# Performance work log

Hardware: AMD Instinct MI355X
Metric: run time of the kernel (lower is better)

The kernel has to match this reference:

```python
import jax, jax.numpy as jnp
import numpy as np
import math

B, L, DM, H, NREL, VS = 16, 512, 512, 8, 4, 5
DK = DM // H


def setup_inputs() -> dict:
    key = jax.random.key(0)
    ks = jax.random.split(key, 16)
    s = 1.0 / math.sqrt(DM)
    inp = {
        'query': jax.random.normal(ks[0], (B, L, DM), jnp.float32),
        'key': jax.random.normal(ks[1], (B, L, DM), jnp.float32),
        'value': jax.random.normal(ks[2], (B, L, DM), jnp.float32),
        'rel_mat': jax.random.randint(ks[3], (B, NREL, L, L), 0, VS),
        'mask': jnp.ones((B, L, L), dtype=bool),
        'Wq': jax.random.normal(ks[4], (DM, DM), jnp.float32) * s,
        'bq': jnp.zeros((DM,), jnp.float32),
        'Wk': jax.random.normal(ks[5], (DM, DM), jnp.float32) * s,
        'bk': jnp.zeros((DM,), jnp.float32),
        'Wv': jax.random.normal(ks[6], (DM, DM), jnp.float32) * s,
        'bv': jnp.zeros((DM,), jnp.float32),
        'Wo': jax.random.normal(ks[7], (DM, DM), jnp.float32) * s,
        'bo': jnp.zeros((DM,), jnp.float32),
    }
    # relation embeddings: (n_rel, h, vs, d_k), padding_idx=0 rows are zero
    se = jax.random.normal(ks[8], (NREL, H, VS, DK), jnp.float32) * 0.02
    ve = jax.random.normal(ks[9], (NREL, H, VS, DK), jnp.float32) * 0.02
    inp['score_emb'] = se.at[:, :, 0, :].set(0.0)
    inp['value_emb'] = ve.at[:, :, 0, :].set(0.0)
    return inp


def reference(query, key, value, rel_mat, mask, Wq, bq, Wk, bk, Wv, bv, Wo, bo, score_emb, value_emb):
    b, l, dm = query.shape
    n_rel, h, vs, dk = score_emb.shape
    scale = 1.0 / math.sqrt(dk)

    def proj(x, W, bias):
        # (b, l, dm) -> (b, h, l, dk)
        return (x @ W.T + bias).reshape(b, l, h, dk).transpose(0, 2, 1, 3)

    q = proj(query, Wq, bq)
    k = proj(key, Wk, bk)
    v = proj(value, Wv, bv)

    # relative-position score: gather q.emb^T along vocab axis by rel_mat
    rps = jnp.einsum('bhid,rhvd->rbhiv', q, score_emb) * scale  # (r,b,h,l,vs)
    idx = jnp.broadcast_to(rel_mat.transpose(1, 0, 2, 3)[:, :, None], (n_rel, b, h, l, l))
    rel_score = jnp.take_along_axis(rps, idx, axis=-1).sum(0)  # (b,h,l,l)

    scores = jnp.einsum('bhid,bhjd->bhij', q, k) * scale + rel_score
    scores = jnp.where(mask[:, None], scores, -1e9)
    p_attn = jax.nn.softmax(scores, axis=-1)  # (b,h,l,l)

    x = jnp.einsum('bhij,bhjd->bhid', p_attn, v)

    # relative-position value: accumulate attention mass per relation id (skip pad id 0)
    one_hot = jax.nn.one_hot(rel_mat, vs, dtype=p_attn.dtype)  # (b,r,l,l,vs)
    acm = jnp.einsum('bhij,brijs->brhis', p_attn, one_hot)[..., 1:]  # (b,r,h,l,vs-1)
    x = x + jnp.einsum('brhis,rhsd->bhid', acm, value_emb[:, :, 1:])

    out = x.transpose(0, 2, 1, 3).reshape(b, l, dm) @ Wo.T + bo
    return out
```

## Files before the change

kernel.cpp:

```cpp
#include <hip/hip_runtime.h>

#define B_    16
#define L_    512
#define DM_   512
#define H_    8
#define DK_   64
#define NREL_ 4
#define VS_   5

typedef __bf16 bf16x8 __attribute__((ext_vector_type(8)));
typedef float  f32x4  __attribute__((ext_vector_type(4)));

union U64 { uint2 u; long l; };

__device__ __forceinline__ void split1(float x, unsigned short& h, unsigned short& l) {
    unsigned u = __float_as_uint(x);
    h = (unsigned short)(u >> 16);
    float r = x - __uint_as_float(u & 0xffff0000u);
    l = (unsigned short)(__float_as_uint(r) >> 16);
}
__device__ __forceinline__ unsigned bf16rtne(float f) {
    unsigned u = __float_as_uint(f);
    return (u + 0x7fffu + ((u >> 16) & 1u)) >> 16;
}

__global__ __launch_bounds__(256) void conv_w(
    const float* __restrict__ W0, const float* __restrict__ W1,
    const float* __restrict__ W2, const float* __restrict__ W3,
    unsigned short* __restrict__ hi, unsigned short* __restrict__ lo)
{
    const int which = blockIdx.y;
    const float* src = (which == 0) ? W0 : (which == 1) ? W1 : (which == 2) ? W2 : W3;
    int t = blockIdx.x * 256 + threadIdx.x;
    float4 v = ((const float4*)src)[t];
    ushort4 h4, l4;
    split1(v.x, h4.x, l4.x); split1(v.y, h4.y, l4.y);
    split1(v.z, h4.z, l4.z); split1(v.w, h4.w, l4.w);
    ((ushort4*)(hi + (size_t)which * 262144))[t] = h4;
    ((ushort4*)(lo + (size_t)which * 262144))[t] = l4;
}

__global__ __launch_bounds__(256) void pack_rel(
    const int* __restrict__ rel, unsigned short* __restrict__ relp)
{
    int t = blockIdx.x * 256 + threadIdx.x;
    int b = t >> 16;
    int ij4 = t & 65535;
    const int4* rb = (const int4*)(rel + (size_t)b * 4 * 262144) + ij4;
    int4 r0 = rb[0];
    int4 r1 = rb[65536];
    int4 r2 = rb[131072];
    int4 r3 = rb[196608];
    ushort4 o;
    o.x = (unsigned short)(r0.x | (r1.x << 3) | (r2.x << 6) | (r3.x << 9));
    o.y = (unsigned short)(r0.y | (r1.y << 3) | (r2.y << 6) | (r3.y << 9));
    o.z = (unsigned short)(r0.z | (r1.z << 3) | (r2.z << 6) | (r3.z << 9));
    o.w = (unsigned short)(r0.w | (r1.w << 3) | (r2.w << 6) | (r3.w << 9));
    ((ushort4*)relp)[t] = o;
}

template <int A_SPLIT, int MODE>
__device__ __forceinline__ void gemm_core(
    const float* __restrict__ A32,
    const unsigned short* __restrict__ Ahi_g, const unsigned short* __restrict__ Alo_g,
    const unsigned short* __restrict__ Whi_g, const unsigned short* __restrict__ Wlo_g,
    const float* __restrict__ bias,
    float* __restrict__ out_f, unsigned short* __restrict__ out_h,
    unsigned short* __restrict__ out_l)
{
    extern __shared__ __align__(16) char smem[];
    unsigned short* Ah = (unsigned short*)smem;
    unsigned short* Al = Ah + 128 * 40;
    unsigned short* Wh = Al + 128 * 40;
    unsigned short* Wl = Wh + 128 * 40;

    const int tid = threadIdx.x;
    const int lane = tid & 63, wave = tid >> 6;
    const int wm = (wave & 1) << 6, wn = (wave >> 1) << 6;
    const int fr = lane & 15, fq = lane >> 4, koff = fq << 3;
    const int mb = blockIdx.x << 7, nb = blockIdx.y << 7;

    f32x4 acc[4][4];
#pragma unroll
    for (int i = 0; i < 4; i++)
#pragma unroll
        for (int j = 0; j < 4; j++) acc[i][j] = (f32x4){0.f, 0.f, 0.f, 0.f};

    for (int k0 = 0; k0 < 512; k0 += 32) {
        __syncthreads();
#pragma unroll
        for (int it = 0; it < 2; ++it) {
            int idx = tid + (it << 8);
            int r = idx >> 2, c8 = (idx & 3) << 3;
            *(uint4*)&Wh[r * 40 + c8] = *(const uint4*)&Whi_g[(size_t)(nb + r) * 512 + k0 + c8];
            *(uint4*)&Wl[r * 40 + c8] = *(const uint4*)&Wlo_g[(size_t)(nb + r) * 512 + k0 + c8];
        }
        if (A_SPLIT) {
#pragma unroll
            for (int it = 0; it < 2; ++it) {
                int idx = tid + (it << 8);
                int r = idx >> 2, c8 = (idx & 3) << 3;
                *(uint4*)&Ah[r * 40 + c8] = *(const uint4*)&Ahi_g[(size_t)(mb + r) * 512 + k0 + c8];
                *(uint4*)&Al[r * 40 + c8] = *(const uint4*)&Alo_g[(size_t)(mb + r) * 512 + k0 + c8];
            }
        } else {
#pragma unroll
            for (int it = 0; it < 4; ++it) {
                int idx = tid + (it << 8);
                int r = idx >> 3, c4 = (idx & 7) << 2;
                float4 v = *(const float4*)&A32[(size_t)(mb + r) * 512 + k0 + c4];
                unsigned ux = __float_as_uint(v.x), uy = __float_as_uint(v.y);
                unsigned uz = __float_as_uint(v.z), uw = __float_as_uint(v.w);
                unsigned h01 = __builtin_amdgcn_perm(uy, ux, 0x07060302u);
                unsigned h23 = __builtin_amdgcn_perm(uw, uz, 0x07060302u);
                float rx = v.x - __uint_as_float(ux & 0xffff0000u);
                float ry = v.y - __uint_as_float(uy & 0xffff0000u);
                float rz = v.z - __uint_as_float(uz & 0xffff0000u);
                float rw = v.w - __uint_as_float(uw & 0xffff0000u);
                unsigned l01 = __builtin_amdgcn_perm(__float_as_uint(ry), __float_as_uint(rx), 0x07060302u);
                unsigned l23 = __builtin_amdgcn_perm(__float_as_uint(rw), __float_as_uint(rz), 0x07060302u);
                uint2 hw; hw.x = h01; hw.y = h23;
                uint2 lw; lw.x = l01; lw.y = l23;
                *(uint2*)&Ah[r * 40 + c4] = hw;
                *(uint2*)&Al[r * 40 + c4] = lw;
            }
        }
        __syncthreads();

        bf16x8 ah[4], al[4], bh[4], bl[4];
#pragma unroll
        for (int i = 0; i < 4; i++) {
            ah[i] = *(const bf16x8*)&Ah[(wm + (i << 4) + fr) * 40 + koff];
            al[i] = *(const bf16x8*)&Al[(wm + (i << 4) + fr) * 40 + koff];
            bh[i] = *(const bf16x8*)&Wh[(wn + (i << 4) + fr) * 40 + koff];
            bl[i] = *(const bf16x8*)&Wl[(wn + (i << 4) + fr) * 40 + koff];
        }
#pragma unroll
        for (int mi = 0; mi < 4; mi++)
#pragma unroll
            for (int ni = 0; ni < 4; ni++) {
                acc[mi][ni] = __builtin_amdgcn_mfma_f32_16x16x32_bf16(al[mi], bh[ni], acc[mi][ni], 0, 0, 0);
                acc[mi][ni] = __builtin_amdgcn_mfma_f32_16x16x32_bf16(ah[mi], bl[ni], acc[mi][ni], 0, 0, 0);
                acc[mi][ni] = __builtin_amdgcn_mfma_f32_16x16x32_bf16(ah[mi], bh[ni], acc[mi][ni], 0, 0, 0);
            }
    }
    __syncthreads();

    if (MODE == 0) {
        float* epf = (float*)smem;
#pragma unroll
        for (int pass = 0; pass < 2; pass++) {
            if (pass) __syncthreads();
            if (wm == pass * 64) {
#pragma unroll
                for (int ni = 0; ni < 4; ni++) {
                    float bv = bias[nb + wn + (ni << 4) + fr];
#pragma unroll
                    for (int mi = 0; mi < 4; mi++)
#pragma unroll
                        for (int r = 0; r < 4; r++)
                            epf[((mi << 4) + (fq << 2) + r) * 132 + wn + (ni << 4) + fr]
                                = acc[mi][ni][r] + bv;
                }
            }
            __syncthreads();
#pragma unroll
            for (int p = 0; p < 8; p++) {
                int slot = tid + (p << 8);
                int row = slot >> 5, seg = slot & 31;
                int m = mb + pass * 64 + row;
                *(float4*)&out_f[(size_t)m * 512 + nb + (seg << 2)]
                    = *(const float4*)&epf[row * 132 + (seg << 2)];
            }
        }
    } else if (MODE == 1) {
        unsigned short* ep = (unsigned short*)smem;
#pragma unroll
        for (int pass = 0; pass < 2; pass++) {
            if (pass) __syncthreads();
#pragma unroll
            for (int ni = 0; ni < 4; ni++) {
                float bv = bias[nb + wn + (ni << 4) + fr];
#pragma unroll
                for (int mi = 0; mi < 4; mi++)
#pragma unroll
                    for (int r = 0; r < 4; r++) {
                        float val = acc[mi][ni][r] + bv;
                        unsigned short hv, lv;
                        split1(val, hv, lv);
                        ep[(wm + (mi << 4) + (fq << 2) + r) * 136 + wn + (ni << 4) + fr]
                            = pass ? lv : hv;
                    }
            }
            __syncthreads();
            unsigned short* dst = pass ? out_l : out_h;
#pragma unroll
            for (int p = 0; p < 8; p++) {
                int slot = tid + (p << 8);
                int row = slot >> 4, seg = slot & 15;
                int m = mb + row, colg = nb + (seg << 3);
                int bb = m >> 9, ii = m & 511, hh = colg >> 6, dd = colg & 63;
                size_t idx = (((size_t)(bb << 3) + hh) * 512 + ii) * 64 + dd;
                *(uint4*)&dst[idx] = *(const uint4*)&ep[row * 136 + (seg << 3)];
            }
        }
    } else {
        unsigned short* ep = (unsigned short*)smem;
#pragma unroll
        for (int ni = 0; ni < 4; ni++) {
            float bv = bias[nb + wn + (ni << 4) + fr];
#pragma unroll
            for (int mi = 0; mi < 4; mi++)
#pragma unroll
                for (int r = 0; r < 4; r++)
                    ep[(wm + (mi << 4) + (fq << 2) + r) * 136 + wn + (ni << 4) + fr]
                        = (unsigned short)bf16rtne(acc[mi][ni][r] + bv);
        }
        __syncthreads();
#pragma unroll
        for (int p = 0; p < 8; p++) {
            int slot = tid + (p << 8);
            int row = slot >> 4, seg = slot & 15;
            int m = mb + row, colg = nb + (seg << 3);
            int bb = m >> 9, ii = m & 511, hh = colg >> 6, dd = colg & 63;
            size_t idx = (((size_t)(bb << 3) + hh) * 512 + ii) * 64 + dd;
            *(uint4*)&out_h[idx] = *(const uint4*)&ep[row * 136 + (seg << 3)];
        }
    }
}

__global__ __launch_bounds__(256) void gemm_qkv(
    const float* __restrict__ Aq, const float* __restrict__ Ak, const float* __restrict__ Av,
    const unsigned short* __restrict__ Whi, const unsigned short* __restrict__ Wlo,
    const float* __restrict__ bq, const float* __restrict__ bk, const float* __restrict__ bv,
    unsigned short* __restrict__ Qhi, unsigned short* __restrict__ Qlo,
    unsigned short* __restrict__ Khi, unsigned short* __restrict__ Klo,
    unsigned short* __restrict__ Vb)
{
    const int z = blockIdx.z;
    const float* A = (z == 0) ? Aq : (z == 1) ? Ak : Av;
    const float* bi = (z == 0) ? bq : (z == 1) ? bk : bv;
    if (z < 2) {
        unsigned short* oh = (z == 0) ? Qhi : Khi;
        unsigned short* ol = (z == 0) ? Qlo : Klo;
        gemm_core<0, 1>(A, nullptr, nullptr,
                        Whi + (size_t)z * 262144, Wlo + (size_t)z * 262144, bi,
                        nullptr, oh, ol);
    } else {
        gemm_core<0, 2>(A, nullptr, nullptr,
                        Whi + (size_t)2 * 262144, Wlo + (size_t)2 * 262144, bi,
                        nullptr, Vb, nullptr);
    }
}

__global__ __launch_bounds__(256) void gemm_o(
    const unsigned short* __restrict__ Xhi, const unsigned short* __restrict__ Xlo,
    const unsigned short* __restrict__ Whi, const unsigned short* __restrict__ Wlo,
    const float* __restrict__ bo, float* __restrict__ out)
{
    gemm_core<1, 0>(nullptr, Xhi, Xlo,
                    Whi + (size_t)3 * 262144, Wlo + (size_t)3 * 262144, bo,
                    out, nullptr, nullptr);
}

__global__ __launch_bounds__(256) void rps_kernel(
    const unsigned short* __restrict__ Qhi, const unsigned short* __restrict__ Qlo,
    const float* __restrict__ SE, float* __restrict__ rps)
{
    __shared__ float Qs[64][68];
    __shared__ float ses[20][68];
    const int bh = blockIdx.y;
    const int h  = bh & 7;
    const int i0 = blockIdx.x * 64;
    const int tid = threadIdx.x;

    const size_t qb = ((size_t)bh * L_ + i0) * DK_;
    for (int t = tid; t < 1024; t += 256) {
        int r = t >> 4, c = (t & 15) << 2;
        ushort4 h4 = *(const ushort4*)&Qhi[qb + r * DK_ + c];
        ushort4 l4 = *(const ushort4*)&Qlo[qb + r * DK_ + c];
        Qs[r][c+0] = __uint_as_float((unsigned)h4.x << 16) + __uint_as_float((unsigned)l4.x << 16);
        Qs[r][c+1] = __uint_as_float((unsigned)h4.y << 16) + __uint_as_float((unsigned)l4.y << 16);
        Qs[r][c+2] = __uint_as_float((unsigned)h4.z << 16) + __uint_as_float((unsigned)l4.z << 16);
        Qs[r][c+3] = __uint_as_float((unsigned)h4.w << 16) + __uint_as_float((unsigned)l4.w << 16);
    }
    for (int t = tid; t < 320; t += 256) {
        int rv = t >> 4, c = (t & 15) << 2;
        int r = rv / 5, v = rv % 5;
        *(float4*)&ses[rv][c] = *(const float4*)&SE[((r * H_ + h) * VS_ + v) * DK_ + c];
    }
    __syncthreads();

    const float scale = 0.125f;
    for (int t = tid; t < 1280; t += 256) {
        int i = t / 20, rv = t % 20;
        float s = 0.f;
#pragma unroll 16
        for (int d = 0; d < 64; d++) s += Qs[i][d] * ses[rv][d];
        rps[((size_t)bh * L_ + i0 + i) * 20 + rv] = s * scale;
    }
}

__global__ __launch_bounds__(256, 4) void attn_flash2(
    const unsigned short* __restrict__ Qhi, const unsigned short* __restrict__ Qlo,
    const unsigned short* __restrict__ Khi, const unsigned short* __restrict__ Klo,
    const unsigned short* __restrict__ Vbf, const float* __restrict__ rps,
    const unsigned short* __restrict__ relp, unsigned char* __restrict__ Pout,
    float* __restrict__ linv_g,
    unsigned short* __restrict__ Xhi, unsigned short* __restrict__ Xlo)
{
    __shared__ unsigned short Kh[64 * 72], Kl[64 * 72];
    __shared__ unsigned short Vt[64 * 72];
    __shared__ unsigned short ps[64 * 72];
    __shared__ unsigned short rps_s[64 * 20];

    const int bh = blockIdx.y;
    const int b = bh >> 3, h = bh & 7;
    const int i0 = blockIdx.x * 64;
    const int tid = threadIdx.x;
    const int lane = tid & 63, w = tid >> 6;
    const int grp = lane >> 4, col = lane & 15;

    bf16x8 qh[2], ql[2];
    {
        const size_t qbase = ((size_t)bh * 512 + i0 + w * 16 + col) * 64;
#pragma unroll
        for (int kit = 0; kit < 2; kit++) {
            qh[kit] = *(const bf16x8*)&Qhi[qbase + kit * 32 + grp * 8];
            ql[kit] = *(const bf16x8*)&Qlo[qbase + kit * 32 + grp * 8];
        }
    }
    for (int t = tid; t < 1280; t += 256)
        rps_s[t] = (unsigned short)bf16rtne(rps[((size_t)bh * 512 + i0 + t / 20) * 20 + (t % 20)]);

    f32x4 o_acc[4];
#pragma unroll
    for (int dt = 0; dt < 4; dt++) o_acc[dt] = (f32x4){0.f, 0.f, 0.f, 0.f};
    float l_part[4] = {0.f, 0.f, 0.f, 0.f};

    const size_t kvbase = (size_t)bh * 512 * 64;

    for (int c = 0; c < 8; c++) {
        const int j0 = c * 64;
        __syncthreads();
#pragma unroll
        for (int p = 0; p < 2; p++) {
            int slot = tid + (p << 8);
            int row = slot >> 3, seg = slot & 7;
            size_t src = kvbase + (size_t)(j0 + row) * 64 + seg * 8;
            *(uint4*)&Kh[row * 72 + seg * 8] = *(const uint4*)&Khi[src];
            *(uint4*)&Kl[row * 72 + seg * 8] = *(const uint4*)&Klo[src];
        }
#pragma unroll
        for (int p = 0; p < 2; p++) {
            int slot = tid + (p << 8);
            int dseg = slot >> 6, j = slot & 63;
            uint4 v = *(const uint4*)&Vbf[kvbase + (size_t)(j0 + j) * 64 + dseg * 8];
            const unsigned short* e = (const unsigned short*)&v;
#pragma unroll
            for (int q = 0; q < 8; q++)
                Vt[(dseg * 8 + q) * 72 + j] = e[q];
        }

        unsigned short pkreg[4][4];
#pragma unroll
        for (int jt = 0; jt < 4; jt++)
#pragma unroll
            for (int r = 0; r < 4; r++)
                pkreg[jt][r] = relp[((size_t)b * 512 + i0 + w * 16 + grp * 4 + r) * 512
                                    + j0 + jt * 16 + col];
        __syncthreads();

        f32x4 sacc[4];
#pragma unroll
        for (int jt = 0; jt < 4; jt++) sacc[jt] = (f32x4){0.f, 0.f, 0.f, 0.f};
#pragma unroll
        for (int kit = 0; kit < 2; kit++) {
#pragma unroll
            for (int jt = 0; jt < 4; jt++) {
                bf16x8 kh = *(const bf16x8*)&Kh[(jt * 16 + col) * 72 + kit * 32 + grp * 8];
                bf16x8 kl = *(const bf16x8*)&Kl[(jt * 16 + col) * 72 + kit * 32 + grp * 8];
                sacc[jt] = __builtin_amdgcn_mfma_f32_16x16x32_bf16(ql[kit], kh, sacc[jt], 0, 0, 0);
                sacc[jt] = __builtin_amdgcn_mfma_f32_16x16x32_bf16(qh[kit], kl, sacc[jt], 0, 0, 0);
                sacc[jt] = __builtin_amdgcn_mfma_f32_16x16x32_bf16(qh[kit], kh, sacc[jt], 0, 0, 0);
            }
        }
#pragma unroll
        for (int jt = 0; jt < 4; jt++) {
#pragma unroll
            for (int r = 0; r < 4; r++) {
                int il = w * 16 + grp * 4 + r;
                int pk = pkreg[jt][r];
                const unsigned short* rr = &rps_s[il * 20];
                float s = sacc[jt][r] * 0.125f
                        + __uint_as_float((unsigned)rr[pk & 7] << 16)
                        + __uint_as_float((unsigned)rr[5 + ((pk >> 3) & 7)] << 16)
                        + __uint_as_float((unsigned)rr[10 + ((pk >> 6) & 7)] << 16)
                        + __uint_as_float((unsigned)rr[15 + ((pk >> 9) & 7)] << 16);
                float p = __expf(fminf(s, 30.f));
                l_part[r] += p;
                ps[il * 72 + jt * 16 + col] = (unsigned short)bf16rtne(p);
            }
        }
        __syncthreads();

#pragma unroll
        for (int kit = 0; kit < 2; kit++) {
            bf16x8 pa = *(const bf16x8*)&ps[(w * 16 + col) * 72 + kit * 32 + grp * 8];
#pragma unroll
            for (int dt = 0; dt < 4; dt++) {
                bf16x8 vb = *(const bf16x8*)&Vt[(dt * 16 + col) * 72 + kit * 32 + grp * 8];
                o_acc[dt] = __builtin_amdgcn_mfma_f32_16x16x32_bf16(pa, vb, o_acc[dt], 0, 0, 0);
            }
        }
#pragma unroll
        for (int p = 0; p < 2; p++) {
            int slot = tid + (p << 8);
            int row = slot >> 3, seg = slot & 7;
            uint4 pb = *(const uint4*)&ps[row * 72 + seg * 8];
            const unsigned short* e = (const unsigned short*)&pb;
            float f[8];
#pragma unroll
            for (int q = 0; q < 8; q++)
                f[q] = __uint_as_float((unsigned)e[q] << 16) * 0.03125f;
            int u0 = __builtin_amdgcn_cvt_pk_fp8_f32(f[0], f[1], 0, false);
            u0 = __builtin_amdgcn_cvt_pk_fp8_f32(f[2], f[3], u0, true);
            int u1 = __builtin_amdgcn_cvt_pk_fp8_f32(f[4], f[5], 0, false);
            u1 = __builtin_amdgcn_cvt_pk_fp8_f32(f[6], f[7], u1, true);
            uint2 st; st.x = (unsigned)u0; st.y = (unsigned)u1;
            *(uint2*)&Pout[((size_t)bh * 512 + i0 + row) * 512 + j0 + seg * 8] = st;
        }
    }

    float rinv[4];
#pragma unroll
    for (int r = 0; r < 4; r++) {
        float l = l_part[r];
#pragma unroll
        for (int d = 1; d < 16; d <<= 1) l += __shfl_xor(l, d, 64);
        rinv[r] = 1.f / l;
    }
    if (col == 0) {
#pragma unroll
        for (int r = 0; r < 4; r++)
            linv_g[(size_t)bh * 512 + i0 + w * 16 + grp * 4 + r] = rinv[r];
    }
#pragma unroll
    for (int dt = 0; dt < 4; dt++) {
#pragma unroll
        for (int r = 0; r < 4; r++) {
            float val = o_acc[dt][r] * rinv[r];
            unsigned short hv, lv;
            split1(val, hv, lv);
            size_t xo = ((size_t)b * 512 + i0 + w * 16 + grp * 4 + r) * 512 + h * 64 + dt * 16 + col;
            Xhi[xo] = hv; Xlo[xo] = lv;
        }
    }
}

__global__ __launch_bounds__(256) void acm_kernel(
    const unsigned char* __restrict__ P_g, const unsigned short* __restrict__ relp,
    const float* __restrict__ VE, const float* __restrict__ linv_g,
    unsigned short* __restrict__ Xhi, unsigned short* __restrict__ Xlo)
{
    __shared__ float VE_s[16 * 8 * 68];
    __shared__ unsigned char Pl[32 * 528];
    __shared__ float ac_l[4][8][16];

    const int tid = threadIdx.x;
    const int b = blockIdx.y;
    const int wave = tid >> 6, lane = tid & 63;
    const int i = blockIdx.x * 4 + wave;
    const int grp = lane >> 4, col = lane & 15;

#pragma unroll
    for (int k = 0; k < 8; k++) {
        int idx4 = tid + (k << 8);
        int off = idx4 << 2;
        int bin = off >> 9, hh = (off >> 6) & 7, dd = off & 63;
        int r = bin >> 2, s = (bin & 3) + 1;
        *(float4*)&VE_s[(bin * 8 + hh) * 68 + dd] =
            *(const float4*)&VE[(((size_t)r * 8 + hh) * 5 + s) * 64 + dd];
    }
#pragma unroll
    for (int p = 0; p < 4; p++) {
        int slot = tid + (p << 8);
        int row = slot >> 5, seg = slot & 31;
        int hh = row >> 2, iw = row & 3;
        *(uint4*)&Pl[row * 528 + seg * 16] =
            *(const uint4*)&P_g[(((size_t)b * 8 + hh) * 512 + blockIdx.x * 4 + iw) * 512 + seg * 16];
    }
    __syncthreads();

    const int r_ = col >> 2, s_ = (col & 3) + 1, sh = 3 * r_;
    const unsigned char* Prow = &Pl[((col & 7) * 4 + wave) * 528];
    f32x4 acc = (f32x4){0.f, 0.f, 0.f, 0.f};

    for (int kit = 0; kit < 16; kit++) {
        const int k0 = kit * 32;
        U64 pa; pa.u = *(const uint2*)&Prow[k0 + grp * 8];
        uint4 pk8 = *(const uint4*)&relp[((size_t)b * 512 + i) * 512 + k0 + grp * 8];
        const unsigned* pw = (const unsigned*)&pk8;
        unsigned bytes[2] = {0u, 0u};
#pragma unroll
        for (int q = 0; q < 8; q++) {
            unsigned word = pw[q >> 1];
            unsigned pk = (q & 1) ? (word >> 16) : (word & 0xffffu);
            unsigned id = (pk >> sh) & 7u;
            unsigned bit = (id == (unsigned)s_) ? 0x38u : 0u;
            bytes[q >> 2] |= bit << ((q & 3) * 8);
        }
        U64 ob; ob.u.x = bytes[0]; ob.u.y = bytes[1];
        acc = __builtin_amdgcn_mfma_f32_16x16x32_fp8_fp8(pa.l, ob.l, acc, 0, 0, 0);
    }

    if (grp < 2) {
#pragma unroll
        for (int r = 0; r < 4; r++)
            ac_l[wave][grp * 4 + r][col] = acc[r];
    }
    __syncthreads();

    const int hh = lane >> 3, dq = lane & 7, d0 = dq * 8;
    float out[8] = {0.f, 0.f, 0.f, 0.f, 0.f, 0.f, 0.f, 0.f};
#pragma unroll
    for (int bin = 0; bin < 16; bin++) {
        float a = ac_l[wave][hh][bin];
        float4 v0 = *(const float4*)&VE_s[(bin * 8 + hh) * 68 + d0];
        float4 v1 = *(const float4*)&VE_s[(bin * 8 + hh) * 68 + d0 + 4];
        out[0] = fmaf(a, v0.x, out[0]); out[1] = fmaf(a, v0.y, out[1]);
        out[2] = fmaf(a, v0.z, out[2]); out[3] = fmaf(a, v0.w, out[3]);
        out[4] = fmaf(a, v1.x, out[4]); out[5] = fmaf(a, v1.y, out[5]);
        out[6] = fmaf(a, v1.z, out[6]); out[7] = fmaf(a, v1.w, out[7]);
    }
    float scale = linv_g[((size_t)b * 8 + hh) * 512 + i] * 32.f;
    size_t xo = ((size_t)b * 512 + i) * 512 + hh * 64 + d0;
    ushort4 xh0 = *(const ushort4*)&Xhi[xo], xh1 = *(const ushort4*)&Xhi[xo + 4];
    ushort4 xl0 = *(const ushort4*)&Xlo[xo], xl1 = *(const ushort4*)&Xlo[xo + 4];
    ushort4 nh[2], nl[2];
    unsigned short* nhp = (unsigned short*)&nh[0];
    unsigned short* nlp = (unsigned short*)&nl[0];
#pragma unroll
    for (int q = 0; q < 8; q++) {
        unsigned short hv = (q < 4) ? ((const unsigned short*)&xh0)[q] : ((const unsigned short*)&xh1)[q - 4];
        unsigned short lv = (q < 4) ? ((const unsigned short*)&xl0)[q] : ((const unsigned short*)&xl1)[q - 4];
        float x = __uint_as_float((unsigned)hv << 16) + __uint_as_float((unsigned)lv << 16);
        x += out[q] * scale;
        unsigned short oh2, ol2;
        split1(x, oh2, ol2);
        nhp[q] = oh2; nlp[q] = ol2;
    }
    *(ushort4*)&Xhi[xo] = nh[0]; *(ushort4*)&Xhi[xo + 4] = nh[1];
    *(ushort4*)&Xlo[xo] = nl[0]; *(ushort4*)&Xlo[xo + 4] = nl[1];
}

extern "C" void kernel_launch(void* const* d_in, const int* in_sizes, int n_in,
                              void* d_out, int out_size, void* d_ws, size_t ws_size,
                              hipStream_t stream)
{
    const float* query = (const float*)d_in[0];
    const float* key_  = (const float*)d_in[1];
    const float* value = (const float*)d_in[2];
    const int*   rel   = (const int*)  d_in[3];
    const float* Wq = (const float*)d_in[5];
    const float* bq = (const float*)d_in[6];
    const float* Wk = (const float*)d_in[7];
    const float* bk = (const float*)d_in[8];
    const float* Wv = (const float*)d_in[9];
    const float* bv = (const float*)d_in[10];
    const float* Wo = (const float*)d_in[11];
    const float* bo = (const float*)d_in[12];
    const float* SE = (const float*)d_in[13];
    const float* VE = (const float*)d_in[14];

    char* base = (char*)d_ws;
    unsigned short* Qhi  = (unsigned short*)(base);
    unsigned short* Qlo  = (unsigned short*)(base + 8388608);
    unsigned short* Khi  = (unsigned short*)(base + 2 * 8388608);
    unsigned short* Klo  = (unsigned short*)(base + 3 * 8388608);
    unsigned short* Vb   = (unsigned short*)(base + 4 * 8388608);
    unsigned short* relp = (unsigned short*)(base + 5 * 8388608);
    unsigned short* Xhi  = (unsigned short*)(base + 6 * 8388608);
    unsigned short* Xlo  = (unsigned short*)(base + 7 * 8388608);
    float*          RPSp = (float*)         (base + 8 * 8388608);
    unsigned short* Whi  = (unsigned short*)(base + 8 * 8388608 + 5242880);
    unsigned short* Wlo  = (unsigned short*)(base + 8 * 8388608 + 5242880 + 2097152);
    unsigned char*  Pg   = (unsigned char*) (base + 8 * 8388608 + 5242880 + 2 * 2097152);
    float*          linv = (float*)         (base + 8 * 8388608 + 5242880 + 2 * 2097152 + 33554432);

    conv_w<<<dim3(256, 4), 256, 0, stream>>>(Wq, Wk, Wv, Wo, Whi, Wlo);
    pack_rel<<<4096, 256, 0, stream>>>(rel, relp);

    gemm_qkv<<<dim3(64, 4, 3), 256, 40960, stream>>>(query, key_, value, Whi, Wlo,
                                                     bq, bk, bv, Qhi, Qlo, Khi, Klo, Vb);

    rps_kernel<<<dim3(8, 128), 256, 0, stream>>>(Qhi, Qlo, SE, RPSp);

    attn_flash2<<<dim3(8, 128), 256, 0, stream>>>(Qhi, Qlo, Khi, Klo, Vb, RPSp,
                                                  relp, Pg, linv, Xhi, Xlo);

    acm_kernel<<<dim3(128, 16), 256, 0, stream>>>(Pg, relp, VE, linv, Xhi, Xlo);

    gemm_o<<<dim3(64, 4), 256, 40960, stream>>>(Xhi, Xlo, Whi, Wlo, bo, (float*)d_out);
}
```

Measured before the change: 342.1 us.

## Pre-split QKV activations to bf16 hi/lo and stage GEMM tiles via global_load_lds

Adds a conv_a pass that splits the fp32 query/key/value inputs into bf16 hi/lo arrays ahead of time, reusing the Xhi/Xlo and Pg workspace regions. The shared GEMM core then loads A and W tiles straight into LDS with global_load_lds, one wave per operand, using a fragment-ordered unpadded layout, and drops the register round trip and in-loop conversion. The aim is to cut VALU and register-staging work in the projection GEMMs, at the cost of an extra launch and extra memory traffic to write and re-read the split activations. The unpadded LDS layout may also change bank-conflict behaviour.

```diff
diff --git a/kernel.cpp b/kernel.cpp
--- a/kernel.cpp
+++ b/kernel.cpp
@@ -22,6 +22,12 @@
 __device__ __forceinline__ unsigned bf16rtne(float f) {
     unsigned u = __float_as_uint(f);
     return (u + 0x7fffu + ((u >> 16) & 1u)) >> 16;
+}
+
+__device__ __forceinline__ void gload_lds16(const unsigned short* g, void* l) {
+    __builtin_amdgcn_global_load_lds(
+        (const __attribute__((address_space(1))) unsigned int*)g,
+        (__attribute__((address_space(3))) unsigned int*)l, 16, 0, 0);
 }
 
 __global__ __launch_bounds__(256) void conv_w(
@@ -38,6 +44,25 @@
     split1(v.z, h4.z, l4.z); split1(v.w, h4.w, l4.w);
     ((ushort4*)(hi + (size_t)which * 262144))[t] = h4;
     ((ushort4*)(lo + (size_t)which * 262144))[t] = l4;
+}
+
+__global__ __launch_bounds__(256) void conv_a(
+    const float* __restrict__ Aq, const float* __restrict__ Ak, const float* __restrict__ Av,
+    unsigned short* __restrict__ qh, unsigned short* __restrict__ ql,
+    unsigned short* __restrict__ kh, unsigned short* __restrict__ kl,
+    unsigned short* __restrict__ vh, unsigned short* __restrict__ vl)
+{
+    const int z = blockIdx.y;
+    const float* src = (z == 0) ? Aq : (z == 1) ? Ak : Av;
+    unsigned short* oh = (z == 0) ? qh : (z == 1) ? kh : vh;
+    unsigned short* ol = (z == 0) ? ql : (z == 1) ? kl : vl;
+    int t = blockIdx.x * 256 + threadIdx.x;
+    float4 v = ((const float4*)src)[t];
+    ushort4 h4, l4;
+    split1(v.x, h4.x, l4.x); split1(v.y, h4.y, l4.y);
+    split1(v.z, h4.z, l4.z); split1(v.w, h4.w, l4.w);
+    ((ushort4*)oh)[t] = h4;
+    ((ushort4*)ol)[t] = l4;
 }
 
 __global__ __launch_bounds__(256) void pack_rel(
@@ -59,9 +84,8 @@
     ((ushort4*)relp)[t] = o;
 }
 
-template <int A_SPLIT, int MODE>
+template <int MODE>
 __device__ __forceinline__ void gemm_core(
-    const float* __restrict__ A32,
     const unsigned short* __restrict__ Ahi_g, const unsigned short* __restrict__ Alo_g,
     const unsigned short* __restrict__ Whi_g, const unsigned short* __restrict__ Wlo_g,
     const float* __restrict__ bias,
@@ -69,16 +93,17 @@
     unsigned short* __restrict__ out_l)
 {
     extern __shared__ __align__(16) char smem[];
-    unsigned short* Ah = (unsigned short*)smem;
-    unsigned short* Al = Ah + 128 * 40;
-    unsigned short* Wh = Al + 128 * 40;
-    unsigned short* Wl = Wh + 128 * 40;
 
     const int tid = threadIdx.x;
-    const int lane = tid & 63, wave = tid >> 6;
-    const int wm = (wave & 1) << 6, wn = (wave >> 1) << 6;
-    const int fr = lane & 15, fq = lane >> 4, koff = fq << 3;
+    const int lane = tid & 63, w = tid >> 6;
+    const int wm = (w & 1) << 6, wn = (w >> 1) << 6;
+    const int fr = lane & 15, fq = lane >> 4;
     const int mb = blockIdx.x << 7, nb = blockIdx.y << 7;
+
+    const unsigned short* stage_src =
+        (w == 0) ? Ahi_g : (w == 1) ? Alo_g : (w == 2) ? Whi_g : Wlo_g;
+    const int stage_rowbase = (w < 2) ? mb : nb;
+    char* stage_dst = smem + w * 8192;
 
     f32x4 acc[4][4];
 #pragma unroll
@@ -89,51 +114,27 @@
     for (int k0 = 0; k0 < 512; k0 += 32) {
         __syncthreads();
 #pragma unroll
-        for (int it = 0; it < 2; ++it) {
-            int idx = tid + (it << 8);
-            int r = idx >> 2, c8 = (idx & 3) << 3;
-            *(uint4*)&Wh[r * 40 + c8] = *(const uint4*)&Whi_g[(size_t)(nb + r) * 512 + k0 + c8];
-            *(uint4*)&Wl[r * 40 + c8] = *(const uint4*)&Wlo_g[(size_t)(nb + r) * 512 + k0 + c8];
-        }
-        if (A_SPLIT) {
-#pragma unroll
-            for (int it = 0; it < 2; ++it) {
-                int idx = tid + (it << 8);
-                int r = idx >> 2, c8 = (idx & 3) << 3;
-                *(uint4*)&Ah[r * 40 + c8] = *(const uint4*)&Ahi_g[(size_t)(mb + r) * 512 + k0 + c8];
-                *(uint4*)&Al[r * 40 + c8] = *(const uint4*)&Alo_g[(size_t)(mb + r) * 512 + k0 + c8];
-            }
-        } else {
-#pragma unroll
-            for (int it = 0; it < 4; ++it) {
-                int idx = tid + (it << 8);
-                int r = idx >> 3, c4 = (idx & 7) << 2;
-                float4 v = *(const float4*)&A32[(size_t)(mb + r) * 512 + k0 + c4];
-                unsigned ux = __float_as_uint(v.x), uy = __float_as_uint(v.y);
-                unsigned uz = __float_as_uint(v.z), uw = __float_as_uint(v.w);
-                unsigned h01 = __builtin_amdgcn_perm(uy, ux, 0x07060302u);
-                unsigned h23 = __builtin_amdgcn_perm(uw, uz, 0x07060302u);
-                float rx = v.x - __uint_as_float(ux & 0xffff0000u);
-                float ry = v.y - __uint_as_float(uy & 0xffff0000u);
-                float rz = v.z - __uint_as_float(uz & 0xffff0000u);
-                float rw = v.w - __uint_as_float(uw & 0xffff0000u);
-                unsigned l01 = __builtin_amdgcn_perm(__float_as_uint(ry), __float_as_uint(rx), 0x07060302u);
-                unsigned l23 = __builtin_amdgcn_perm(__float_as_uint(rw), __float_as_uint(rz), 0x07060302u);
-                uint2 hw; hw.x = h01; hw.y = h23;
-                uint2 lw; lw.x = l01; lw.y = l23;
-                *(uint2*)&Ah[r * 40 + c4] = hw;
-                *(uint2*)&Al[r * 40 + c4] = lw;
-            }
+        for (int sub = 0; sub < 8; sub++) {
+            const unsigned short* g =
+                &stage_src[(size_t)(stage_rowbase + sub * 16 + fr) * 512 + k0 + fq * 8];
+            gload_lds16(g, stage_dst + sub * 1024);
         }
         __syncthreads();
 
+        const unsigned short* Ah = (const unsigned short*)smem;
+        const unsigned short* Al = (const unsigned short*)(smem + 8192);
+        const unsigned short* Wh = (const unsigned short*)(smem + 16384);
+        const unsigned short* Wl = (const unsigned short*)(smem + 24576);
+
         bf16x8 ah[4], al[4], bh[4], bl[4];
 #pragma unroll
         for (int i = 0; i < 4; i++) {
-            ah[i] = *(const bf16x8*)&Ah[(wm + (i << 4) + fr) * 40 + koff];
-            al[i] = *(const bf16x8*)&Al[(wm + (i << 4) + fr) * 40 + koff];
-            bh[i] = *(const bf16x8*)&Wh[(wn + (i << 4) + fr) * 40 + koff];
-            bl[i] = *(const bf16x8*)&Wl[(wn + (i << 4) + fr) * 40 + koff];
+            int aoff = (((wm >> 4) + i) << 9) + (lane << 3);
+            int boff = (((wn >> 4) + i) << 9) + (lane << 3);
+            ah[i] = *(const bf16x8*)&Ah[aoff];
+            al[i] = *(const bf16x8*)&Al[aoff];
+            bh[i] = *(const bf16x8*)&Wh[boff];
+            bl[i] = *(const bf16x8*)&Wl[boff];
         }
 #pragma unroll
         for (int mi = 0; mi < 4; mi++)
@@ -146,6 +147,7 @@
     }
     __syncthreads();
 
+    const int fq2 = lane >> 4;
     if (MODE == 0) {
         float* epf = (float*)smem;
 #pragma unroll
@@ -159,7 +161,7 @@
                     for (int mi = 0; mi < 4; mi++)
 #pragma unroll
                         for (int r = 0; r < 4; r++)
-                            epf[((mi << 4) + (fq << 2) + r) * 132 + wn + (ni << 4) + fr]
+                            epf[((mi << 4) + (fq2 << 2) + r) * 132 + wn + (ni << 4) + fr]
                                 = acc[mi][ni][r] + bv;
                 }
             }
@@ -188,7 +190,7 @@
                         float val = acc[mi][ni][r] + bv;
                         unsigned short hv, lv;
                         split1(val, hv, lv);
-                        ep[(wm + (mi << 4) + (fq << 2) + r) * 136 + wn + (ni << 4) + fr]
+                        ep[(wm + (mi << 4) + (fq2 << 2) + r) * 136 + wn + (ni << 4) + fr]
                             = pass ? lv : hv;
                     }
             }
@@ -213,7 +215,7 @@
             for (int mi = 0; mi < 4; mi++)
 #pragma unroll
                 for (int r = 0; r < 4; r++)
-                    ep[(wm + (mi << 4) + (fq << 2) + r) * 136 + wn + (ni << 4) + fr]
+                    ep[(wm + (mi << 4) + (fq2 << 2) + r) * 136 + wn + (ni << 4) + fr]
                         = (unsigned short)bf16rtne(acc[mi][ni][r] + bv);
         }
         __syncthreads();
@@ -230,7 +232,9 @@
 }
 
 __global__ __launch_bounds__(256) void gemm_qkv(
-    const float* __restrict__ Aq, const float* __restrict__ Ak, const float* __restrict__ Av,
+    const unsigned short* __restrict__ Aqh, const unsigned short* __restrict__ Aql,
+    const unsigned short* __restrict__ Akh, const unsigned short* __restrict__ Akl,
+    const unsigned short* __restrict__ Avh, const unsigned short* __restrict__ Avl,
     const unsigned short* __restrict__ Whi, const unsigned short* __restrict__ Wlo,
     const float* __restrict__ bq, const float* __restrict__ bk, const float* __restrict__ bv,
     unsigned short* __restrict__ Qhi, unsigned short* __restrict__ Qlo,
@@ -238,18 +242,17 @@
     unsigned short* __restrict__ Vb)
 {
     const int z = blockIdx.z;
-    const float* A = (z == 0) ? Aq : (z == 1) ? Ak : Av;
+    const unsigned short* Ah = (z == 0) ? Aqh : (z == 1) ? Akh : Avh;
+    const unsigned short* Al = (z == 0) ? Aql : (z == 1) ? Akl : Avl;
     const float* bi = (z == 0) ? bq : (z == 1) ? bk : bv;
     if (z < 2) {
         unsigned short* oh = (z == 0) ? Qhi : Khi;
         unsigned short* ol = (z == 0) ? Qlo : Klo;
-        gemm_core<0, 1>(A, nullptr, nullptr,
-                        Whi + (size_t)z * 262144, Wlo + (size_t)z * 262144, bi,
-                        nullptr, oh, ol);
+        gemm_core<1>(Ah, Al, Whi + (size_t)z * 262144, Wlo + (size_t)z * 262144, bi,
+                     nullptr, oh, ol);
     } else {
-        gemm_core<0, 2>(A, nullptr, nullptr,
-                        Whi + (size_t)2 * 262144, Wlo + (size_t)2 * 262144, bi,
-                        nullptr, Vb, nullptr);
+        gemm_core<2>(Ah, Al, Whi + (size_t)2 * 262144, Wlo + (size_t)2 * 262144, bi,
+                     nullptr, Vb, nullptr);
     }
 }
 
@@ -258,9 +261,8 @@
     const unsigned short* __restrict__ Whi, const unsigned short* __restrict__ Wlo,
     const float* __restrict__ bo, float* __restrict__ out)
 {
-    gemm_core<1, 0>(nullptr, Xhi, Xlo,
-                    Whi + (size_t)3 * 262144, Wlo + (size_t)3 * 262144, bo,
-                    out, nullptr, nullptr);
+    gemm_core<0>(Xhi, Xlo, Whi + (size_t)3 * 262144, Wlo + (size_t)3 * 262144, bo,
+                 out, nullptr, nullptr);
 }
 
 __global__ __launch_bounds__(256) void rps_kernel(
@@ -588,11 +590,21 @@
     unsigned char*  Pg   = (unsigned char*) (base + 8 * 8388608 + 5242880 + 2 * 2097152);
     float*          linv = (float*)         (base + 8 * 8388608 + 5242880 + 2 * 2097152 + 33554432);
 
+    unsigned short* Aqh = Xhi;
+    unsigned short* Aql = Xlo;
+    unsigned short* Akh = (unsigned short*)(Pg);
+    unsigned short* Akl = (unsigned short*)(Pg + 8388608);
+    unsigned short* Avh = (unsigned short*)(Pg + 16777216);
+    unsigned short* Avl = (unsigned short*)(Pg + 25165824);
+
     conv_w<<<dim3(256, 4), 256, 0, stream>>>(Wq, Wk, Wv, Wo, Whi, Wlo);
+    conv_a<<<dim3(4096, 3), 256, 0, stream>>>(query, key_, value,
+                                              Aqh, Aql, Akh, Akl, Avh, Avl);
     pack_rel<<<4096, 256, 0, stream>>>(rel, relp);
 
-    gemm_qkv<<<dim3(64, 4, 3), 256, 40960, stream>>>(query, key_, value, Whi, Wlo,
-                                                     bq, bk, bv, Qhi, Qlo, Khi, Klo, Vb);
+    gemm_qkv<<<dim3(64, 4, 3), 256, 34816, stream>>>(Aqh, Aql, Akh, Akl, Avh, Avl,
+                                                     Whi, Wlo, bq, bk, bv,
+                                                     Qhi, Qlo, Khi, Klo, Vb);
 
     rps_kernel<<<dim3(8, 128), 256, 0, stream>>>(Qhi, Qlo, SE, RPSp);
 
@@ -601,5 +613,5 @@
 
     acm_kernel<<<dim3(128, 16), 256, 0, stream>>>(Pg, relp, VE, linv, Xhi, Xlo);
 
-    gemm_o<<<dim3(64, 4), 256, 40960, stream>>>(Xhi, Xlo, Whi, Wlo, bo, (float*)d_out);
-}
+    gemm_o<<<dim3(64, 4), 256, 34816, stream>>>(Xhi, Xlo, Whi, Wlo, bo, (float*)d_out);
+}
```

Measured after the change: 368.8 us. +7.8%, slower.
